# Kernel tuning notes

Measured on AMD Instinct MI355X. Metric: run time of the kernel, lower is better.

## Reference

```python
import jax, jax.numpy as jnp
import numpy as np

B, D, L, T, K = 16, 256, 256, 1000, 3
DW, DC = 4, 2  # dim_w, dim_c
CH = 8         # ConvSwishBlock out channels (10 = 1 start + 1 end + 8)


def swish(x):
    return x * jax.nn.sigmoid(x)


def setup_inputs() -> dict:
    key = jax.random.key(0)
    ks = jax.random.split(key, 12)
    # durations ~ U[1,6] per phone -> sum ~ 3.5*L ~ 896 <= T
    durations = 1.0 + 5.0 * jax.random.uniform(ks[0], (B, L), dtype=jnp.float32)
    phoneme = jax.random.normal(ks[1], (B, D, L), dtype=jnp.float32)
    # True = padded phone position
    phone_len = L - (jnp.arange(B) % 4) * 16
    phoneme_mask = (jnp.arange(L)[None, :] >= phone_len[:, None])[:, None, :]
    durations = jnp.where(phoneme_mask[:, 0, :], 0.0, durations)
    s = 0.02
    p = {
        'proj_w_W': s * jax.random.normal(ks[2], (D, D)), 'proj_w_b': jnp.zeros((D,)),
        'conv_w_W': s * jax.random.normal(ks[3], (CH, D, K)), 'conv_w_b': jnp.zeros((CH,)),
        'mlp_w_W': s * jax.random.normal(ks[4], (2 + CH, DW)), 'mlp_w_b': jnp.zeros((DW,)),
        'lin_w_W': s * jax.random.normal(ks[5], (D * DW, D)), 'lin_w_b': jnp.zeros((D,)),
        'proj_c_W': s * jax.random.normal(ks[6], (D, D)), 'proj_c_b': jnp.zeros((D,)),
        'conv_c_W': s * jax.random.normal(ks[7], (CH, D, K)), 'conv_c_b': jnp.zeros((CH,)),
        'mlp_c_W': s * jax.random.normal(ks[8], (2 + CH, DC)), 'mlp_c_b': jnp.zeros((DC,)),
        'lin_c_W': s * jax.random.normal(ks[9], (DW * DC, D)), 'lin_c_b': jnp.zeros((D,)),
    }
    return {'durations': durations, 'phoneme': phoneme, 'phoneme_mask': phoneme_mask, **p}


def _conv_branch(x, phone_pad, projW, projb, convW, convb):
    # x: (B, D, L). 1x1 conv projection, then K-wide 'same' conv to CH channels, swish, mask.
    x = jnp.einsum('od,bdl->bol', projW, x) + projb[None, :, None]
    h = jax.lax.conv_general_dilated(x, convW, (1,), 'SAME',
                                     dimension_numbers=('NCH', 'OIH', 'NCH'))
    h = swish(h + convb[None, :, None])
    h = jnp.where(phone_pad[:, None, :], 0.0, h)
    return h.transpose(0, 2, 1)  # (B, L, CH)


def _forward(durations, phoneme, phoneme_mask,
             proj_w_W, proj_w_b, conv_w_W, conv_w_b, mlp_w_W, mlp_w_b, lin_w_W, lin_w_b,
             proj_c_W, proj_c_b, conv_c_W, conv_c_b, mlp_c_W, mlp_c_b, lin_c_W, lin_c_b):
    phone_pad = phoneme_mask[:, 0, :]                       # (B, L) True = pad
    frame_len = jnp.clip(jnp.round(jnp.sum(durations, -1)), 0, T).astype(jnp.int32)
    frame_pad = jnp.arange(T)[None, :] >= frame_len[:, None]  # (B, T) True = pad
    attn_pad = frame_pad[:, :, None] | phone_pad[:, None, :]  # (B, T, L)

    sd = jnp.cumsum(durations, -1)                          # (B, L) cumulative end times
    sk = sd - durations                                     # (B, L) start times
    t = jnp.arange(1, T + 1, dtype=durations.dtype)
    S = jnp.where(attn_pad, 0.0, t[None, :, None] - sk[:, None, :])                    # (B,T,L)
    E = jnp.where(attn_pad, 0.0, jnp.broadcast_to(sd[:, None, :], attn_pad.shape)
                  - sk[:, None, :])                                                    # (B,T,L)

    # W branch: per-(frame, phone) attention weights over phones
    h_w = _conv_branch(phoneme, phone_pad, proj_w_W, proj_w_b, conv_w_W, conv_w_b)     # (B,L,CH)
    feat_w = jnp.concatenate(
        [S[..., None], E[..., None], jnp.broadcast_to(h_w[:, None], (B, T, L, CH))], -1)
    w = swish(feat_w @ mlp_w_W + mlp_w_b)                   # (B, T, L, DW)
    w = jnp.where(phone_pad[:, None, :, None], -jnp.inf, w)
    w = jax.nn.softmax(w, axis=2)                           # softmax over phones
    w = jnp.where(frame_pad[:, :, None, None], 0.0, w)

    # C branch: auxiliary per-(frame, phone) context
    h_c = _conv_branch(phoneme, phone_pad, proj_c_W, proj_c_b, conv_c_W, conv_c_b)
    feat_c = jnp.concatenate(
        [S[..., None], E[..., None], jnp.broadcast_to(h_c[:, None], (B, T, L, CH))], -1)
    c = swish(feat_c @ mlp_c_W + mlp_c_b)                   # (B, T, L, DC)

    # combine: wh = einsum over phones with phoneme features, wc with c matrix
    wh = jnp.einsum('btnq,bnh->btqh', w, phoneme.transpose(0, 2, 1))  # (B,T,DW,D)
    wh = wh.reshape(B, T, DW * D) @ lin_w_W + lin_w_b                 # (B,T,D)
    wc = jnp.einsum('btnq,btnp->btqp', w, c)                          # (B,T,DW,DC)
    wc = wc.reshape(B, T, DW * DC) @ lin_c_W + lin_c_b                # (B,T,D)
    return wh + wc


def reference(durations, phoneme, phoneme_mask,
              proj_w_W, proj_w_b, conv_w_W, conv_w_b, mlp_w_W, mlp_w_b, lin_w_W, lin_w_b,
              proj_c_W, proj_c_b, conv_c_W, conv_c_b, mlp_c_W, mlp_c_b, lin_c_W, lin_c_b):
    return _forward(durations, phoneme, phoneme_mask,
                    proj_w_W, proj_w_b, conv_w_W, conv_w_b, mlp_w_W, mlp_w_b, lin_w_W, lin_w_b,
                    proj_c_W, proj_c_b, conv_c_W, conv_c_b, mlp_c_W, mlp_c_b, lin_c_W, lin_c_b)
```

## Files before the change

kernel.cpp:

```cpp
#include <hip/hip_runtime.h>


typedef short v8s __attribute__((ext_vector_type(8)));
typedef _Float16 v8h __attribute__((ext_vector_type(8)));
typedef float f4 __attribute__((ext_vector_type(4)));

__device__ __forceinline__ float bf2f(unsigned short h) {
  return __uint_as_float(((unsigned int)h) << 16);
}
__device__ __forceinline__ unsigned short f2bf(float f) {
  unsigned int u = __float_as_uint(f);
  u = (u + 0x7FFFu + ((u >> 16) & 1u)) >> 16;
  return (unsigned short)u;
}
__device__ __forceinline__ float swishf(float x) {
  return x * __builtin_amdgcn_rcpf(1.f + __expf(-x));
}

__global__ __launch_bounds__(256) void k_prep(
    const float* __restrict__ dur, const float* __restrict__ ph,
    const float* __restrict__ liWw,
    const float* __restrict__ cvWw, const float* __restrict__ pjWw,
    const float* __restrict__ pjbw,
    const float* __restrict__ cvWc, const float* __restrict__ pjWc,
    const float* __restrict__ pjbc,
    float* __restrict__ sk, int* __restrict__ frame_len,
    unsigned short* __restrict__ Mb, float* __restrict__ bK,
    unsigned short* __restrict__ LWT, unsigned short* __restrict__ phT) {
  __shared__ float sm[32 * 33];
  int blk = blockIdx.x, tid = threadIdx.x;
  if (blk < 16) {
    int b = blk, l = tid;
    float d = dur[b * 256 + l];
    sm[l] = d;
    __syncthreads();
    for (int off = 1; off < 256; off <<= 1) {
      float v = (l >= off) ? sm[l - off] : 0.f;
      __syncthreads();
      sm[l] += v;
      __syncthreads();
    }
    sk[b * 256 + l] = sm[l] - d;
    if (l == 255) {
      int fl = (int)rintf(sm[255]);
      frame_len[b] = min(max(fl, 0), 1000);
    }
  } else if (blk < 64) {
    int x = blk - 16;
    int br = x / 24, ck = x % 24;
    int ch = ck / 3, k = ck % 3;
    const float* convW = br ? cvWc : cvWw;
    const float* projW = br ? pjWc : pjWw;
    const float* projb = br ? pjbc : pjbw;
    int d = tid;
    float acc = 0.f;
    for (int o = 0; o < 256; o++)
      acc += convW[ch * 768 + o * 3 + k] * projW[o * 256 + d];
    Mb[(br * 24 + ck) * 256 + d] = f2bf(acc);
    if (d == 0) {
      float bb = 0.f;
      for (int o = 0; o < 256; o++)
        bb += convW[ch * 768 + o * 3 + k] * projb[o];
      bK[br * 24 + ck] = bb;
    }
  } else if (blk < 320) {
    int idx = blk - 64;
    int kt = idx & 31, ot = idx >> 5;
    int tx = tid & 31, ty = tid >> 5;
#pragma unroll
    for (int r = 0; r < 4; r++) {
      int row = ty + r * 8;
      sm[row * 33 + tx] = liWw[(size_t)(kt * 32 + row) * 256 + ot * 32 + tx];
    }
    __syncthreads();
#pragma unroll
    for (int r = 0; r < 4; r++) {
      int row = ty + r * 8;
      LWT[(size_t)(ot * 32 + row) * 1024 + kt * 32 + tx] =
          f2bf(sm[tx * 33 + row]);
    }
  } else {
    int idx = blk - 320;
    int ht = idx & 7, lt = (idx >> 3) & 7, b = idx >> 6;
    int tx = tid & 31, ty = tid >> 5;
#pragma unroll
    for (int r = 0; r < 4; r++) {
      int row = ty + r * 8;
      sm[row * 33 + tx] =
          ph[(size_t)b * 65536 + (size_t)(ht * 32 + row) * 256 + lt * 32 + tx];
    }
    __syncthreads();
#pragma unroll
    for (int r = 0; r < 4; r++) {
      int row = ty + r * 8;
      phT[(size_t)b * 65536 + (size_t)(lt * 32 + row) * 256 + ht * 32 + tx] =
          f2bf(sm[tx * 33 + row]);
    }
  }
}

__global__ __launch_bounds__(256) void k_convG(
    const unsigned short* __restrict__ phT, const unsigned short* __restrict__ Mb,
    const float* __restrict__ bK, const float* __restrict__ cvbw,
    const float* __restrict__ cvbc, const float* __restrict__ dur,
    const unsigned short* __restrict__ LWT,
    float* __restrict__ hw, float* __restrict__ hc,
    _Float16* __restrict__ G) {
  __shared__ __align__(16) float C[256 * 49];
  int blk = blockIdx.x;
  int tid = threadIdx.x, wave = tid >> 6, lane = tid & 63;
  int quad = lane >> 4, col = lane & 15;
  if (blk < 16) {
    int b = blk;
    int l0 = wave * 64;
    const unsigned short* Ab = phT + (size_t)b * 65536;
    f4 acc[4][3] = {};
#pragma unroll
    for (int k0 = 0; k0 < 256; k0 += 32) {
      v8s af[4], bf[3];
#pragma unroll
      for (int lt = 0; lt < 4; lt++)
        af[lt] = *(const v8s*)(Ab + (size_t)(l0 + lt * 16 + col) * 256 + k0 + quad * 8);
#pragma unroll
      for (int ct = 0; ct < 3; ct++)
        bf[ct] = *(const v8s*)(Mb + (size_t)(ct * 16 + col) * 256 + k0 + quad * 8);
#pragma unroll
      for (int lt = 0; lt < 4; lt++)
#pragma unroll
        for (int ct = 0; ct < 3; ct++)
          acc[lt][ct] = __builtin_amdgcn_mfma_f32_16x16x32_bf16(af[lt], bf[ct],
                                                                acc[lt][ct], 0, 0, 0);
    }
#pragma unroll
    for (int lt = 0; lt < 4; lt++)
#pragma unroll
      for (int ct = 0; ct < 3; ct++)
#pragma unroll
        for (int r = 0; r < 4; r++)
          C[(l0 + lt * 16 + quad * 4 + r) * 49 + ct * 16 + col] = acc[lt][ct][r];
    __syncthreads();
    int l = tid;
    float dv = dur[b * 256 + l];
    bool vld = (dv != 0.f);
#pragma unroll
    for (int br = 0; br < 2; br++) {
      const float* convb = br ? cvbc : cvbw;
      float* dst = br ? hc : hw;
#pragma unroll
      for (int ch = 0; ch < 8; ch++) {
        int ck = br * 24 + ch * 3;
        float v = convb[ch] + bK[ck + 1] + C[l * 49 + ck + 1];
        if (l > 0) v += bK[ck + 0] + C[(l - 1) * 49 + ck + 0];
        if (l < 255) v += bK[ck + 2] + C[(l + 1) * 49 + ck + 2];
        v = swishf(v);
        dst[((size_t)(b * 256 + l)) * 8 + ch] = vld ? v : 0.f;
      }
    }
  } else {
    int idx = blk - 16;
    int b = idx >> 4;
    int sub = idx & 15;
    int q = sub >> 2, quadr = sub & 3;
    int mo = (quadr >> 1) * 128, nl = (quadr & 1) * 128;
    int wm = (wave & 1) * 64, wn = (wave >> 1) * 64;
    const unsigned short* Ag = LWT + (size_t)q * 256;
    const unsigned short* Bg = phT + (size_t)b * 65536;
    f4 acc[4][4] = {};
#pragma unroll
    for (int k0 = 0; k0 < 256; k0 += 32) {
      v8s af[4], bf[4];
#pragma unroll
      for (int mt = 0; mt < 4; mt++)
        af[mt] = *(const v8s*)(Ag + (size_t)(mo + wm + mt * 16 + col) * 1024 +
                               k0 + quad * 8);
#pragma unroll
      for (int nt = 0; nt < 4; nt++)
        bf[nt] = *(const v8s*)(Bg + (size_t)(nl + wn + nt * 16 + col) * 256 +
                               k0 + quad * 8);
#pragma unroll
      for (int mt = 0; mt < 4; mt++)
#pragma unroll
        for (int nt = 0; nt < 4; nt++)
          acc[mt][nt] = __builtin_amdgcn_mfma_f32_16x16x32_bf16(af[mt], bf[nt],
                                                                acc[mt][nt], 0, 0, 0);
    }
    _Float16* Gb = G + (size_t)b * 262144 + q * 256;
#pragma unroll
    for (int mt = 0; mt < 4; mt++)
#pragma unroll
      for (int r = 0; r < 4; r++) {
        int orow = mo + wm + mt * 16 + quad * 4 + r;
#pragma unroll
        for (int nt = 0; nt < 4; nt++) {
          int lcol = nl + wn + nt * 16 + col;
          Gb[(size_t)orow * 1024 + lcol] = (_Float16)acc[mt][nt][r];
        }
      }
  }
}

__global__ __launch_bounds__(256) void k_soft(
    const float* __restrict__ dur, const float* __restrict__ sk,
    const int* __restrict__ frame_len,
    const float* __restrict__ hw, const float* __restrict__ hc,
    const float* __restrict__ mlpWw, const float* __restrict__ mlpbw,
    const float* __restrict__ mlpWc, const float* __restrict__ mlpbc,
    _Float16* __restrict__ w, float* __restrict__ wc) {
  __shared__ __align__(16) float4 Lbw4[272];
  __shared__ __align__(16) float4 Laux4[272];
  __shared__ float4 wredM[4];
  int b = blockIdx.y;
  int t0 = blockIdx.x * 16;
  int tid = threadIdx.x, wave = tid >> 6, lane = tid & 63;

  {
    int l = tid;
    float4 a0 = *(const float4*)&hw[((size_t)(b * 256 + l)) * 8];
    float4 a1 = *(const float4*)&hw[((size_t)(b * 256 + l)) * 8 + 4];
    float4 c0 = *(const float4*)&hc[((size_t)(b * 256 + l)) * 8];
    float4 c1 = *(const float4*)&hc[((size_t)(b * 256 + l)) * 8 + 4];
    float hwv[8] = {a0.x, a0.y, a0.z, a0.w, a1.x, a1.y, a1.z, a1.w};
    float hcv[8] = {c0.x, c0.y, c0.z, c0.w, c1.x, c1.y, c1.z, c1.w};
    float dl = dur[b * 256 + l];
    float skl = sk[b * 256 + l];
    float msk = (dl != 0.f) ? 1.f : 0.f;
    float A[4];
#pragma unroll
    for (int q = 0; q < 4; q++) {
      float a = mlpbw[q] + dl * mlpWw[4 + q] - skl * mlpWw[q];
#pragma unroll
      for (int ch = 0; ch < 8; ch++) a += hwv[ch] * mlpWw[(2 + ch) * 4 + q];
      A[q] = (msk != 0.f) ? a : -1e30f;
    }
    float bb0 = mlpbc[0] + dl * mlpWc[2] - skl * mlpWc[0];
    float bb1 = mlpbc[1] + dl * mlpWc[3] - skl * mlpWc[1];
#pragma unroll
    for (int ch = 0; ch < 8; ch++) {
      bb0 += hcv[ch] * mlpWc[(2 + ch) * 2 + 0];
      bb1 += hcv[ch] * mlpWc[(2 + ch) * 2 + 1];
    }
    int li = l + (l >> 4);
    float4 Av = {A[0], A[1], A[2], A[3]};
    Lbw4[li] = Av;
    float4 xv = {bb0, bb1, msk, 0.f};
    Laux4[li] = xv;
    float m0 = A[0], m1 = A[1], m2 = A[2], m3 = A[3];
#pragma unroll
    for (int off = 1; off < 64; off <<= 1) {
      m0 = fmaxf(m0, __shfl_xor(m0, off));
      m1 = fmaxf(m1, __shfl_xor(m1, off));
      m2 = fmaxf(m2, __shfl_xor(m2, off));
      m3 = fmaxf(m3, __shfl_xor(m3, off));
    }
    if (lane == 0) {
      float4 mv = {m0, m1, m2, m3};
      wredM[wave] = mv;
    }
  }
  __syncthreads();
  float4 W0 = wredM[0], W1 = wredM[1], W2 = wredM[2], W3 = wredM[3];
  float maxA[4] = {fmaxf(fmaxf(W0.x, W1.x), fmaxf(W2.x, W3.x)),
                   fmaxf(fmaxf(W0.y, W1.y), fmaxf(W2.y, W3.y)),
                   fmaxf(fmaxf(W0.z, W1.z), fmaxf(W2.z, W3.z)),
                   fmaxf(fmaxf(W0.w, W1.w), fmaxf(W2.w, W3.w))};

  int fl = frame_len[b];
  int tl = wave * 4 + (lane >> 4);
  int l16 = lane & 15;
  int t = t0 + tl;
  bool live = (t < fl);
  float tp1 = (float)(t + 1);
  float mw0[4] = {mlpWw[0], mlpWw[1], mlpWw[2], mlpWw[3]};
  float mc0 = mlpWc[0], mc1 = mlpWc[1];
  float m[4];
#pragma unroll
  for (int q = 0; q < 4; q++)
    m[q] = live ? fmaxf(maxA[q] + tp1 * mw0[q], 0.f) : 1e30f;

  float s[4] = {}, pw[4][2] = {{}, {}, {}, {}};
  v8h eh[4][2];
  int lbase = l16 * 17;
#pragma unroll
  for (int j = 0; j < 16; j++) {
    float4 A4 = Lbw4[lbase + j];
    float4 ax = Laux4[lbase + j];
    float cp0 = swishf(ax.x + tp1 * mc0);
    float cp1 = swishf(ax.y + tp1 * mc1);
    float Aq[4] = {A4.x, A4.y, A4.z, A4.w};
#pragma unroll
    for (int q = 0; q < 4; q++) {
      float z = Aq[q] + tp1 * mw0[q];
      float e = __expf(swishf(z) - m[q]) * ax.z;
      eh[q][j >> 3][j & 7] = (_Float16)e;
      s[q] += e;
      pw[q][0] += e * cp0;
      pw[q][1] += e * cp1;
    }
  }
#pragma unroll
  for (int off = 1; off < 16; off <<= 1) {
#pragma unroll
    for (int q = 0; q < 4; q++) {
      s[q] += __shfl_xor(s[q], off);
      pw[q][0] += __shfl_xor(pw[q][0], off);
      pw[q][1] += __shfl_xor(pw[q][1], off);
    }
  }
  size_t base = ((size_t)b * 1024 + t) * 1024;
#pragma unroll
  for (int q = 0; q < 4; q++) {
    float iv = live ? __builtin_amdgcn_rcpf(s[q]) : 0.f;
    _Float16 ivh = (_Float16)iv;
    v8h w0 = eh[q][0] * ivh;
    v8h w1 = eh[q][1] * ivh;
    *(v8h*)(w + base + q * 256 + l16 * 16) = w0;
    *(v8h*)(w + base + q * 256 + l16 * 16 + 8) = w1;
    if (l16 == 0 && t < 1000) {
      wc[((size_t)(b * 1000 + t)) * 8 + q * 2 + 0] = pw[q][0] * iv;
      wc[((size_t)(b * 1000 + t)) * 8 + q * 2 + 1] = pw[q][1] * iv;
    }
  }
}

__global__ __launch_bounds__(256) void k_out(const _Float16* __restrict__ w,
                                             const _Float16* __restrict__ G,
                                             const float* __restrict__ lwb,
                                             const float* __restrict__ lcb,
                                             const float* __restrict__ LC,
                                             const float* __restrict__ wc,
                                             float* __restrict__ out) {
  int b = blockIdx.y;
  int t0 = (blockIdx.x >> 1) * 32;
  int o0 = (blockIdx.x & 1) * 128;
  int tid = threadIdx.x, wave = tid >> 6, lane = tid & 63;
  int quad = lane >> 4, col = lane & 15;
  __shared__ __align__(16) _Float16 Asm[32 * 40];
  __shared__ __align__(16) _Float16 Bsm[128 * 40];
  __shared__ float bias_s[128];
  __shared__ float lcs[8][128];
  __shared__ float wcs[32][8];

  for (int i = tid; i < 128; i += 256) bias_s[i] = lwb[o0 + i] + lcb[o0 + i];
  for (int i = tid; i < 1024; i += 256)
    lcs[i >> 7][i & 127] = LC[(i >> 7) * 256 + o0 + (i & 127)];
  {
    int r = tid >> 3, j = tid & 7;
    int t = t0 + r;
    wcs[r][j] = (t < 1000) ? wc[((size_t)(b * 1000 + t)) * 8 + j] : 0.f;
  }

  bool aload = tid < 128;
  int arow = tid >> 2, aseg = tid & 3;
  const _Float16* Ag =
      w + (size_t)b * 1048576 + (size_t)(t0 + arow) * 1024 + aseg * 8;
  _Float16* Al = Asm + arow * 40 + aseg * 8;
  int brow = wave * 32 + (lane >> 2), bseg = lane & 3;
  const _Float16* Bg0 =
      G + (size_t)b * 262144 + (size_t)(o0 + brow) * 1024 + bseg * 8;
  const _Float16* Bg1 = Bg0 + 16 * 1024;
  _Float16* Bl0 = Bsm + brow * 40 + bseg * 8;
  _Float16* Bl1 = Bl0 + 16 * 40;

  int wm = (wave & 1) * 16, wn = (wave >> 1) * 64;
  f4 acc[4] = {};
  uint4 ra = {0, 0, 0, 0};
  if (aload) ra = *(const uint4*)Ag;
  uint4 rb0 = *(const uint4*)Bg0;
  uint4 rb1 = *(const uint4*)Bg1;
  for (int k0 = 0; k0 < 1024; k0 += 32) {
    __syncthreads();
    if (aload) *(uint4*)Al = ra;
    *(uint4*)Bl0 = rb0;
    *(uint4*)Bl1 = rb1;
    __syncthreads();
    if (k0 + 32 < 1024) {
      if (aload) ra = *(const uint4*)(Ag + k0 + 32);
      rb0 = *(const uint4*)(Bg0 + k0 + 32);
      rb1 = *(const uint4*)(Bg1 + k0 + 32);
    }
    v8h af = *(const v8h*)(Asm + (wm + col) * 40 + quad * 8);
    v8h bf[4];
#pragma unroll
    for (int nt = 0; nt < 4; nt++)
      bf[nt] = *(const v8h*)(Bsm + (wn + nt * 16 + col) * 40 + quad * 8);
#pragma unroll
    for (int nt = 0; nt < 4; nt++)
      acc[nt] = __builtin_amdgcn_mfma_f32_16x16x32_f16(af, bf[nt],
                                                       acc[nt], 0, 0, 0);
  }
#pragma unroll
  for (int r = 0; r < 4; r++) {
    int lrow = wm + quad * 4 + r;
    int trow = t0 + lrow;
    if (trow < 1000) {
      float4 wa = *(const float4*)&wcs[lrow][0];
      float4 wb = *(const float4*)&wcs[lrow][4];
      float wcl[8] = {wa.x, wa.y, wa.z, wa.w, wb.x, wb.y, wb.z, wb.w};
#pragma unroll
      for (int nt = 0; nt < 4; nt++) {
        int oc = wn + nt * 16 + col;
        float v = acc[nt][r] + bias_s[oc];
#pragma unroll
        for (int jj = 0; jj < 8; jj++) v = fmaf(wcl[jj], lcs[jj][oc], v);
        out[((size_t)(b * 1000 + trow)) * 256 + o0 + oc] = v;
      }
    }
  }
}

extern "C" void kernel_launch(void* const* d_in, const int* in_sizes, int n_in,
                              void* d_out, int out_size, void* d_ws, size_t ws_size,
                              hipStream_t stream) {
  const float* dur  = (const float*)d_in[0];
  const float* ph   = (const float*)d_in[1];
  const float* pjWw = (const float*)d_in[3];
  const float* pjbw = (const float*)d_in[4];
  const float* cvWw = (const float*)d_in[5];
  const float* cvbw = (const float*)d_in[6];
  const float* mlWw = (const float*)d_in[7];
  const float* mlbw = (const float*)d_in[8];
  const float* liWw = (const float*)d_in[9];
  const float* libw = (const float*)d_in[10];
  const float* pjWc = (const float*)d_in[11];
  const float* pjbc = (const float*)d_in[12];
  const float* cvWc = (const float*)d_in[13];
  const float* cvbc = (const float*)d_in[14];
  const float* mlWc = (const float*)d_in[15];
  const float* mlbc = (const float*)d_in[16];
  const float* liWc = (const float*)d_in[17];
  const float* libc = (const float*)d_in[18];
  float* out = (float*)d_out;

  float* f = (float*)d_ws;
  size_t o = 0;
  float* sk = f + o;            o += 4096;
  int* fl = (int*)(f + o);      o += 16;
  float* bK = f + o;            o += 64;
  unsigned short* Mb = (unsigned short*)(f + o); o += 6144;
  float* hw = f + o;            o += 16 * 256 * 8;
  float* hc = f + o;            o += 16 * 256 * 8;
  float* wc = f + o;            o += 16 * 1000 * 8;
  _Float16* G = (_Float16*)(f + o);              o += 2097152;
  _Float16* w = (_Float16*)(f + o);              o += 8388608;
  unsigned short* phT = (unsigned short*)(f + o); o += 524288;
  unsigned short* LWT = (unsigned short*)(f + o); o += 131072;

  k_prep<<<1344, 256, 0, stream>>>(dur, ph, liWw, cvWw, pjWw, pjbw, cvWc, pjWc,
                                   pjbc, sk, fl, Mb, bK, LWT, phT);
  k_convG<<<272, 256, 0, stream>>>(phT, Mb, bK, cvbw, cvbc, dur, LWT, hw, hc, G);
  k_soft<<<dim3(63, 16), 256, 0, stream>>>(dur, sk, fl, hw, hc, mlWw, mlbw,
                                           mlWc, mlbc, w, wc);
  k_out<<<dim3(64, 16), 256, 0, stream>>>(w, G, libw, libc, liWc, wc, out);
}
```

Measured before the change: 179.3 us.

## Fuse soft-alignment weights into the output GEMM and drop the w buffer

The soft-alignment kernel and the output GEMM kernel are merged. Each block now computes its 32 frame rows of fp16 alignment weights directly into shared memory and multiplies them against G, so the large w intermediate (about 32 MB of fp16) no longer goes through global memory. The per-phone MLP logits and per-batch maxima move into the conv kernel's epilogue, and the bias reduction in prep is parallelised with a wave shuffle. In exchange, each block recomputes the exps for two q-halves, uses more shared memory, and covers all 256 output columns per block, which reduces parallelism per frame tile.

```diff
diff --git a/kernel.cpp b/kernel.cpp
--- a/kernel.cpp
+++ b/kernel.cpp
@@ -53,15 +53,21 @@
     const float* projW = br ? pjWc : pjWw;
     const float* projb = br ? pjbc : pjbw;
     int d = tid;
-    float acc = 0.f;
-    for (int o = 0; o < 256; o++)
-      acc += convW[ch * 768 + o * 3 + k] * projW[o * 256 + d];
-    Mb[(br * 24 + ck) * 256 + d] = f2bf(acc);
-    if (d == 0) {
-      float bb = 0.f;
-      for (int o = 0; o < 256; o++)
-        bb += convW[ch * 768 + o * 3 + k] * projb[o];
-      bK[br * 24 + ck] = bb;
+    float a0 = 0.f, a1 = 0.f, a2 = 0.f, a3 = 0.f;
+    for (int o = 0; o < 256; o += 4) {
+      a0 += convW[ch * 768 + (o + 0) * 3 + k] * projW[(o + 0) * 256 + d];
+      a1 += convW[ch * 768 + (o + 1) * 3 + k] * projW[(o + 1) * 256 + d];
+      a2 += convW[ch * 768 + (o + 2) * 3 + k] * projW[(o + 2) * 256 + d];
+      a3 += convW[ch * 768 + (o + 3) * 3 + k] * projW[(o + 3) * 256 + d];
+    }
+    Mb[(br * 24 + ck) * 256 + d] = f2bf((a0 + a1) + (a2 + a3));
+    if (tid < 64) {
+      float pb = 0.f;
+      for (int o = tid; o < 256; o += 64)
+        pb += convW[ch * 768 + o * 3 + k] * projb[o];
+#pragma unroll
+      for (int off = 1; off < 64; off <<= 1) pb += __shfl_xor(pb, off);
+      if (tid == 0) bK[br * 24 + ck] = pb;
     }
   } else if (blk < 320) {
     int idx = blk - 64;
@@ -103,10 +109,13 @@
     const unsigned short* __restrict__ phT, const unsigned short* __restrict__ Mb,
     const float* __restrict__ bK, const float* __restrict__ cvbw,
     const float* __restrict__ cvbc, const float* __restrict__ dur,
-    const unsigned short* __restrict__ LWT,
-    float* __restrict__ hw, float* __restrict__ hc,
-    _Float16* __restrict__ G) {
+    const float* __restrict__ sk, const float* __restrict__ mlpWw,
+    const float* __restrict__ mlpbw, const float* __restrict__ mlpWc,
+    const float* __restrict__ mlpbc, const unsigned short* __restrict__ LWT,
+    float* __restrict__ Lbw, float* __restrict__ Laux,
+    float* __restrict__ maxAb, _Float16* __restrict__ G) {
   __shared__ __align__(16) float C[256 * 49];
+  __shared__ float redm[4][4];
   int blk = blockIdx.x;
   int tid = threadIdx.x, wave = tid >> 6, lane = tid & 63;
   int quad = lane >> 4, col = lane & 15;
@@ -142,20 +151,57 @@
     int l = tid;
     float dv = dur[b * 256 + l];
     bool vld = (dv != 0.f);
+    float hv[2][8];
 #pragma unroll
     for (int br = 0; br < 2; br++) {
       const float* convb = br ? cvbc : cvbw;
-      float* dst = br ? hc : hw;
 #pragma unroll
       for (int ch = 0; ch < 8; ch++) {
         int ck = br * 24 + ch * 3;
         float v = convb[ch] + bK[ck + 1] + C[l * 49 + ck + 1];
         if (l > 0) v += bK[ck + 0] + C[(l - 1) * 49 + ck + 0];
         if (l < 255) v += bK[ck + 2] + C[(l + 1) * 49 + ck + 2];
-        v = swishf(v);
-        dst[((size_t)(b * 256 + l)) * 8 + ch] = vld ? v : 0.f;
+        hv[br][ch] = vld ? swishf(v) : 0.f;
       }
     }
+    float skl = sk[b * 256 + l];
+    float A[4];
+#pragma unroll
+    for (int q = 0; q < 4; q++) {
+      float a = mlpbw[q] + dv * mlpWw[4 + q] - skl * mlpWw[q];
+#pragma unroll
+      for (int ch = 0; ch < 8; ch++) a += hv[0][ch] * mlpWw[(2 + ch) * 4 + q];
+      A[q] = vld ? a : -1e30f;
+    }
+    float bb0 = mlpbc[0] + dv * mlpWc[2] - skl * mlpWc[0];
+    float bb1 = mlpbc[1] + dv * mlpWc[3] - skl * mlpWc[1];
+#pragma unroll
+    for (int ch = 0; ch < 8; ch++) {
+      bb0 += hv[1][ch] * mlpWc[(2 + ch) * 2 + 0];
+      bb1 += hv[1][ch] * mlpWc[(2 + ch) * 2 + 1];
+    }
+    float4 Av = {A[0], A[1], A[2], A[3]};
+    ((float4*)Lbw)[b * 256 + l] = Av;
+    float4 Xv = {bb0, bb1, vld ? 1.f : 0.f, 0.f};
+    ((float4*)Laux)[b * 256 + l] = Xv;
+    float m0 = A[0], m1 = A[1], m2 = A[2], m3 = A[3];
+#pragma unroll
+    for (int off = 1; off < 64; off <<= 1) {
+      m0 = fmaxf(m0, __shfl_xor(m0, off));
+      m1 = fmaxf(m1, __shfl_xor(m1, off));
+      m2 = fmaxf(m2, __shfl_xor(m2, off));
+      m3 = fmaxf(m3, __shfl_xor(m3, off));
+    }
+    if (lane == 0) {
+      redm[wave][0] = m0;
+      redm[wave][1] = m1;
+      redm[wave][2] = m2;
+      redm[wave][3] = m3;
+    }
+    __syncthreads();
+    if (tid < 4)
+      maxAb[b * 4 + tid] = fmaxf(fmaxf(redm[0][tid], redm[1][tid]),
+                                 fmaxf(redm[2][tid], redm[3][tid]));
   } else {
     int idx = blk - 16;
     int b = idx >> 4;
@@ -199,213 +245,151 @@
   }
 }
 
-__global__ __launch_bounds__(256) void k_soft(
-    const float* __restrict__ dur, const float* __restrict__ sk,
-    const int* __restrict__ frame_len,
-    const float* __restrict__ hw, const float* __restrict__ hc,
-    const float* __restrict__ mlpWw, const float* __restrict__ mlpbw,
-    const float* __restrict__ mlpWc, const float* __restrict__ mlpbc,
-    _Float16* __restrict__ w, float* __restrict__ wc) {
-  __shared__ __align__(16) float4 Lbw4[272];
-  __shared__ __align__(16) float4 Laux4[272];
-  __shared__ float4 wredM[4];
-  int b = blockIdx.y;
-  int t0 = blockIdx.x * 16;
+__global__ __launch_bounds__(256) void k_fuse(
+    const float* __restrict__ Lbw, const float* __restrict__ Laux,
+    const float* __restrict__ maxAb, const int* __restrict__ frame_len,
+    const float* __restrict__ mlpWw, const float* __restrict__ mlpWc,
+    const _Float16* __restrict__ G, const float* __restrict__ lwb,
+    const float* __restrict__ lcb, const float* __restrict__ LC,
+    float* __restrict__ out) {
+  __shared__ __align__(16) _Float16 Asm[32 * 512];
+  __shared__ __align__(16) float4 Lb4[264];
+  __shared__ __align__(16) float4 Lx4[264];
+  __shared__ float bias_s[256];
+  __shared__ float lcs[8][256];
+  __shared__ float wcs[32][8];
+
+  int idx = blockIdx.x;
+  int b = (idx & 7) * 2 + ((idx >> 3) & 1);
+  int t0 = (idx >> 4) * 32;
   int tid = threadIdx.x, wave = tid >> 6, lane = tid & 63;
+  int quad = lane >> 4, col = lane & 15;
 
   {
-    int l = tid;
-    float4 a0 = *(const float4*)&hw[((size_t)(b * 256 + l)) * 8];
-    float4 a1 = *(const float4*)&hw[((size_t)(b * 256 + l)) * 8 + 4];
-    float4 c0 = *(const float4*)&hc[((size_t)(b * 256 + l)) * 8];
-    float4 c1 = *(const float4*)&hc[((size_t)(b * 256 + l)) * 8 + 4];
-    float hwv[8] = {a0.x, a0.y, a0.z, a0.w, a1.x, a1.y, a1.z, a1.w};
-    float hcv[8] = {c0.x, c0.y, c0.z, c0.w, c1.x, c1.y, c1.z, c1.w};
-    float dl = dur[b * 256 + l];
-    float skl = sk[b * 256 + l];
-    float msk = (dl != 0.f) ? 1.f : 0.f;
-    float A[4];
-#pragma unroll
-    for (int q = 0; q < 4; q++) {
-      float a = mlpbw[q] + dl * mlpWw[4 + q] - skl * mlpWw[q];
-#pragma unroll
-      for (int ch = 0; ch < 8; ch++) a += hwv[ch] * mlpWw[(2 + ch) * 4 + q];
-      A[q] = (msk != 0.f) ? a : -1e30f;
-    }
-    float bb0 = mlpbc[0] + dl * mlpWc[2] - skl * mlpWc[0];
-    float bb1 = mlpbc[1] + dl * mlpWc[3] - skl * mlpWc[1];
-#pragma unroll
-    for (int ch = 0; ch < 8; ch++) {
-      bb0 += hcv[ch] * mlpWc[(2 + ch) * 2 + 0];
-      bb1 += hcv[ch] * mlpWc[(2 + ch) * 2 + 1];
-    }
-    int li = l + (l >> 4);
-    float4 Av = {A[0], A[1], A[2], A[3]};
-    Lbw4[li] = Av;
-    float4 xv = {bb0, bb1, msk, 0.f};
-    Laux4[li] = xv;
-    float m0 = A[0], m1 = A[1], m2 = A[2], m3 = A[3];
-#pragma unroll
-    for (int off = 1; off < 64; off <<= 1) {
-      m0 = fmaxf(m0, __shfl_xor(m0, off));
-      m1 = fmaxf(m1, __shfl_xor(m1, off));
-      m2 = fmaxf(m2, __shfl_xor(m2, off));
-      m3 = fmaxf(m3, __shfl_xor(m3, off));
-    }
-    if (lane == 0) {
-      float4 mv = {m0, m1, m2, m3};
-      wredM[wave] = mv;
-    }
+    float4 av = ((const float4*)Lbw)[b * 256 + tid];
+    float4 xv = ((const float4*)Laux)[b * 256 + tid];
+    int li = tid + (tid >> 5);
+    Lb4[li] = av;
+    Lx4[li] = xv;
+    bias_s[tid] = lwb[tid] + lcb[tid];
+#pragma unroll
+    for (int i = 0; i < 8; i++) lcs[i][tid] = LC[i * 256 + tid];
   }
-  __syncthreads();
-  float4 W0 = wredM[0], W1 = wredM[1], W2 = wredM[2], W3 = wredM[3];
-  float maxA[4] = {fmaxf(fmaxf(W0.x, W1.x), fmaxf(W2.x, W3.x)),
-                   fmaxf(fmaxf(W0.y, W1.y), fmaxf(W2.y, W3.y)),
-                   fmaxf(fmaxf(W0.z, W1.z), fmaxf(W2.z, W3.z)),
-                   fmaxf(fmaxf(W0.w, W1.w), fmaxf(W2.w, W3.w))};
-
   int fl = frame_len[b];
-  int tl = wave * 4 + (lane >> 4);
-  int l16 = lane & 15;
-  int t = t0 + tl;
+  float4 mx4 = ((const float4*)maxAb)[b];
+  float mw0 = mlpWw[0], mw1 = mlpWw[1], mw2 = mlpWw[2], mw3 = mlpWw[3];
+  float mc0 = mlpWc[0], mc1 = mlpWc[1];
+
+  int r_loc = lane >> 3, l_grp = lane & 7;
+  int row = wave * 8 + r_loc;
+  int t = t0 + row;
   bool live = (t < fl);
   float tp1 = (float)(t + 1);
-  float mw0[4] = {mlpWw[0], mlpWw[1], mlpWw[2], mlpWw[3]};
-  float mc0 = mlpWc[0], mc1 = mlpWc[1];
-  float m[4];
-#pragma unroll
-  for (int q = 0; q < 4; q++)
-    m[q] = live ? fmaxf(maxA[q] + tp1 * mw0[q], 0.f) : 1e30f;
-
-  float s[4] = {}, pw[4][2] = {{}, {}, {}, {}};
-  v8h eh[4][2];
-  int lbase = l16 * 17;
-#pragma unroll
-  for (int j = 0; j < 16; j++) {
-    float4 A4 = Lbw4[lbase + j];
-    float4 ax = Laux4[lbase + j];
-    float cp0 = swishf(ax.x + tp1 * mc0);
-    float cp1 = swishf(ax.y + tp1 * mc1);
-    float Aq[4] = {A4.x, A4.y, A4.z, A4.w};
-#pragma unroll
-    for (int q = 0; q < 4; q++) {
-      float z = Aq[q] + tp1 * mw0[q];
-      float e = __expf(swishf(z) - m[q]) * ax.z;
-      eh[q][j >> 3][j & 7] = (_Float16)e;
-      s[q] += e;
-      pw[q][0] += e * cp0;
-      pw[q][1] += e * cp1;
+  int rsw = row & 7;
+  int asw = col & 7;
+  int wn = wave * 64;
+  f4 acc[2][4] = {};
+
+  __syncthreads();
+
+#pragma unroll
+  for (int p = 0; p < 2; ++p) {
+    if (p) __syncthreads();
+    float mq0 = p ? mw2 : mw0;
+    float mq1 = p ? mw3 : mw1;
+    float mxa = p ? mx4.z : mx4.x;
+    float mxb = p ? mx4.w : mx4.y;
+    float m0 = live ? fmaxf(mxa + tp1 * mq0, 0.f) : 1e30f;
+    float m1 = live ? fmaxf(mxb + tp1 * mq1, 0.f) : 1e30f;
+    float s0 = 0.f, s1 = 0.f, p00 = 0.f, p01 = 0.f, p10 = 0.f, p11 = 0.f;
+    v8h e0[4], e1[4];
+#pragma unroll
+    for (int j = 0; j < 32; ++j) {
+      int l = l_grp * 32 + j;
+      int li = l + (l >> 5);
+      float4 A4 = Lb4[li];
+      float4 ax = Lx4[li];
+      float cp0 = swishf(ax.x + tp1 * mc0);
+      float cp1 = swishf(ax.y + tp1 * mc1);
+      float Aq0 = p ? A4.z : A4.x;
+      float Aq1 = p ? A4.w : A4.y;
+      float ee0 = __expf(swishf(Aq0 + tp1 * mq0) - m0) * ax.z;
+      float ee1 = __expf(swishf(Aq1 + tp1 * mq1) - m1) * ax.z;
+      e0[j >> 3][j & 7] = (_Float16)ee0;
+      e1[j >> 3][j & 7] = (_Float16)ee1;
+      s0 += ee0;
+      s1 += ee1;
+      p00 += ee0 * cp0;
+      p01 += ee0 * cp1;
+      p10 += ee1 * cp0;
+      p11 += ee1 * cp1;
+    }
+#pragma unroll
+    for (int off = 1; off < 8; off <<= 1) {
+      s0 += __shfl_xor(s0, off);
+      s1 += __shfl_xor(s1, off);
+      p00 += __shfl_xor(p00, off);
+      p01 += __shfl_xor(p01, off);
+      p10 += __shfl_xor(p10, off);
+      p11 += __shfl_xor(p11, off);
+    }
+    float iv0 = live ? __builtin_amdgcn_rcpf(s0) : 0.f;
+    float iv1 = live ? __builtin_amdgcn_rcpf(s1) : 0.f;
+    if (l_grp == 0) {
+      wcs[row][p * 4 + 0] = p00 * iv0;
+      wcs[row][p * 4 + 1] = p01 * iv0;
+      wcs[row][p * 4 + 2] = p10 * iv1;
+      wcs[row][p * 4 + 3] = p11 * iv1;
+    }
+    _Float16 h0 = (_Float16)iv0, h1 = (_Float16)iv1;
+#pragma unroll
+    for (int c = 0; c < 4; ++c) {
+      int sl0 = (l_grp * 4 + c) ^ rsw;
+      int sl1 = 32 + ((l_grp * 4 + c) ^ rsw);
+      *(v8h*)&Asm[(row * 64 + sl0) * 8] = e0[c] * h0;
+      *(v8h*)&Asm[(row * 64 + sl1) * 8] = e1[c] * h1;
+    }
+    __syncthreads();
+    const _Float16* Gp = G + (size_t)b * 262144 + p * 512;
+#pragma unroll 2
+    for (int k0 = 0; k0 < 512; k0 += 32) {
+      int slk = (k0 >> 3) + quad;
+      v8h af0 = *(const v8h*)&Asm[(col * 64 + (slk ^ asw)) * 8];
+      v8h af1 = *(const v8h*)&Asm[((16 + col) * 64 + (slk ^ asw)) * 8];
+      v8h bf[4];
+#pragma unroll
+      for (int nt = 0; nt < 4; ++nt)
+        bf[nt] =
+            *(const v8h*)(Gp + (size_t)(wn + nt * 16 + col) * 1024 + k0 + quad * 8);
+#pragma unroll
+      for (int nt = 0; nt < 4; ++nt) {
+        acc[0][nt] =
+            __builtin_amdgcn_mfma_f32_16x16x32_f16(af0, bf[nt], acc[0][nt], 0, 0, 0);
+        acc[1][nt] =
+            __builtin_amdgcn_mfma_f32_16x16x32_f16(af1, bf[nt], acc[1][nt], 0, 0, 0);
+      }
     }
   }
 #pragma unroll
-  for (int off = 1; off < 16; off <<= 1) {
-#pragma unroll
-    for (int q = 0; q < 4; q++) {
-      s[q] += __shfl_xor(s[q], off);
-      pw[q][0] += __shfl_xor(pw[q][0], off);
-      pw[q][1] += __shfl_xor(pw[q][1], off);
-    }
-  }
-  size_t base = ((size_t)b * 1024 + t) * 1024;
-#pragma unroll
-  for (int q = 0; q < 4; q++) {
-    float iv = live ? __builtin_amdgcn_rcpf(s[q]) : 0.f;
-    _Float16 ivh = (_Float16)iv;
-    v8h w0 = eh[q][0] * ivh;
-    v8h w1 = eh[q][1] * ivh;
-    *(v8h*)(w + base + q * 256 + l16 * 16) = w0;
-    *(v8h*)(w + base + q * 256 + l16 * 16 + 8) = w1;
-    if (l16 == 0 && t < 1000) {
-      wc[((size_t)(b * 1000 + t)) * 8 + q * 2 + 0] = pw[q][0] * iv;
-      wc[((size_t)(b * 1000 + t)) * 8 + q * 2 + 1] = pw[q][1] * iv;
-    }
-  }
-}
-
-__global__ __launch_bounds__(256) void k_out(const _Float16* __restrict__ w,
-                                             const _Float16* __restrict__ G,
-                                             const float* __restrict__ lwb,
-                                             const float* __restrict__ lcb,
-                                             const float* __restrict__ LC,
-                                             const float* __restrict__ wc,
-                                             float* __restrict__ out) {
-  int b = blockIdx.y;
-  int t0 = (blockIdx.x >> 1) * 32;
-  int o0 = (blockIdx.x & 1) * 128;
-  int tid = threadIdx.x, wave = tid >> 6, lane = tid & 63;
-  int quad = lane >> 4, col = lane & 15;
-  __shared__ __align__(16) _Float16 Asm[32 * 40];
-  __shared__ __align__(16) _Float16 Bsm[128 * 40];
-  __shared__ float bias_s[128];
-  __shared__ float lcs[8][128];
-  __shared__ float wcs[32][8];
-
-  for (int i = tid; i < 128; i += 256) bias_s[i] = lwb[o0 + i] + lcb[o0 + i];
-  for (int i = tid; i < 1024; i += 256)
-    lcs[i >> 7][i & 127] = LC[(i >> 7) * 256 + o0 + (i & 127)];
-  {
-    int r = tid >> 3, j = tid & 7;
-    int t = t0 + r;
-    wcs[r][j] = (t < 1000) ? wc[((size_t)(b * 1000 + t)) * 8 + j] : 0.f;
-  }
-
-  bool aload = tid < 128;
-  int arow = tid >> 2, aseg = tid & 3;
-  const _Float16* Ag =
-      w + (size_t)b * 1048576 + (size_t)(t0 + arow) * 1024 + aseg * 8;
-  _Float16* Al = Asm + arow * 40 + aseg * 8;
-  int brow = wave * 32 + (lane >> 2), bseg = lane & 3;
-  const _Float16* Bg0 =
-      G + (size_t)b * 262144 + (size_t)(o0 + brow) * 1024 + bseg * 8;
-  const _Float16* Bg1 = Bg0 + 16 * 1024;
-  _Float16* Bl0 = Bsm + brow * 40 + bseg * 8;
-  _Float16* Bl1 = Bl0 + 16 * 40;
-
-  int wm = (wave & 1) * 16, wn = (wave >> 1) * 64;
-  f4 acc[4] = {};
-  uint4 ra = {0, 0, 0, 0};
-  if (aload) ra = *(const uint4*)Ag;
-  uint4 rb0 = *(const uint4*)Bg0;
-  uint4 rb1 = *(const uint4*)Bg1;
-  for (int k0 = 0; k0 < 1024; k0 += 32) {
-    __syncthreads();
-    if (aload) *(uint4*)Al = ra;
-    *(uint4*)Bl0 = rb0;
-    *(uint4*)Bl1 = rb1;
-    __syncthreads();
-    if (k0 + 32 < 1024) {
-      if (aload) ra = *(const uint4*)(Ag + k0 + 32);
-      rb0 = *(const uint4*)(Bg0 + k0 + 32);
-      rb1 = *(const uint4*)(Bg1 + k0 + 32);
-    }
-    v8h af = *(const v8h*)(Asm + (wm + col) * 40 + quad * 8);
-    v8h bf[4];
-#pragma unroll
-    for (int nt = 0; nt < 4; nt++)
-      bf[nt] = *(const v8h*)(Bsm + (wn + nt * 16 + col) * 40 + quad * 8);
-#pragma unroll
-    for (int nt = 0; nt < 4; nt++)
-      acc[nt] = __builtin_amdgcn_mfma_f32_16x16x32_f16(af, bf[nt],
-                                                       acc[nt], 0, 0, 0);
-  }
-#pragma unroll
-  for (int r = 0; r < 4; r++) {
-    int lrow = wm + quad * 4 + r;
-    int trow = t0 + lrow;
-    if (trow < 1000) {
-      float4 wa = *(const float4*)&wcs[lrow][0];
-      float4 wb = *(const float4*)&wcs[lrow][4];
-      float wcl[8] = {wa.x, wa.y, wa.z, wa.w, wb.x, wb.y, wb.z, wb.w};
-#pragma unroll
-      for (int nt = 0; nt < 4; nt++) {
-        int oc = wn + nt * 16 + col;
-        float v = acc[nt][r] + bias_s[oc];
-#pragma unroll
-        for (int jj = 0; jj < 8; jj++) v = fmaf(wcl[jj], lcs[jj][oc], v);
-        out[((size_t)(b * 1000 + trow)) * 256 + o0 + oc] = v;
+  for (int mt = 0; mt < 2; ++mt)
+#pragma unroll
+    for (int r = 0; r < 4; ++r) {
+      int lrow = mt * 16 + quad * 4 + r;
+      int trow = t0 + lrow;
+      if (trow < 1000) {
+        float4 wa = *(const float4*)&wcs[lrow][0];
+        float4 wb = *(const float4*)&wcs[lrow][4];
+        float wcl[8] = {wa.x, wa.y, wa.z, wa.w, wb.x, wb.y, wb.z, wb.w};
+#pragma unroll
+        for (int nt = 0; nt < 4; ++nt) {
+          int oc = wn + nt * 16 + col;
+          float v = acc[mt][nt][r] + bias_s[oc];
+#pragma unroll
+          for (int jj = 0; jj < 8; ++jj) v = fmaf(wcl[jj], lcs[jj][oc], v);
+          out[((size_t)(b * 1000 + trow)) * 256 + oc] = v;
+        }
       }
     }
-  }
 }
 
 extern "C" void kernel_launch(void* const* d_in, const int* in_sizes, int n_in,
@@ -437,18 +421,17 @@
   int* fl = (int*)(f + o);      o += 16;
   float* bK = f + o;            o += 64;
   unsigned short* Mb = (unsigned short*)(f + o); o += 6144;
-  float* hw = f + o;            o += 16 * 256 * 8;
-  float* hc = f + o;            o += 16 * 256 * 8;
-  float* wc = f + o;            o += 16 * 1000 * 8;
+  float* Lbw = f + o;           o += 16384;
+  float* Laux = f + o;          o += 16384;
+  float* mxA = f + o;           o += 64;
   _Float16* G = (_Float16*)(f + o);              o += 2097152;
-  _Float16* w = (_Float16*)(f + o);              o += 8388608;
   unsigned short* phT = (unsigned short*)(f + o); o += 524288;
   unsigned short* LWT = (unsigned short*)(f + o); o += 131072;
 
   k_prep<<<1344, 256, 0, stream>>>(dur, ph, liWw, cvWw, pjWw, pjbw, cvWc, pjWc,
                                    pjbc, sk, fl, Mb, bK, LWT, phT);
-  k_convG<<<272, 256, 0, stream>>>(phT, Mb, bK, cvbw, cvbc, dur, LWT, hw, hc, G);
-  k_soft<<<dim3(63, 16), 256, 0, stream>>>(dur, sk, fl, hw, hc, mlWw, mlbw,
-                                           mlWc, mlbc, w, wc);
-  k_out<<<dim3(64, 16), 256, 0, stream>>>(w, G, libw, libc, liWc, wc, out);
-}
+  k_convG<<<272, 256, 0, stream>>>(phT, Mb, bK, cvbw, cvbc, dur, sk, mlWw,
+                                   mlbw, mlWc, mlbc, LWT, Lbw, Laux, mxA, G);
+  k_fuse<<<512, 256, 0, stream>>>(Lbw, Laux, mxA, fl, mlWw, mlWc, G, libw,
+                                  libc, liWc, out);
+}
```

Result: faster. 175.6 us (-2.0%).
